# Performance work log

Hardware: AMD Instinct MI355X
Metric: run time of the kernel (lower is better)

## Reference

```python
import jax, jax.numpy as jnp
import numpy as np

B, K, N, D, E, EE, H, P = 512, 64, 1024, 128, 100000, 1024, 256, 12

def setup_inputs() -> dict:
    key = jax.random.key(0)
    ks = jax.random.split(key, 6)
    return {
        'ts_emb': jax.random.normal(ks[0], (B, D, N), jnp.float32),
        'event_table': jax.random.normal(ks[1], (E, EE), jnp.float32),
        'W_t': jax.random.normal(ks[2], (H, EE), jnp.float32) * 0.02,
        'b_t': jnp.zeros((H,), jnp.float32),
        'W_mm': jax.random.normal(ks[3], (P, H + D), jnp.float32) * 0.02,
        'b_mm': jnp.zeros((P,), jnp.float32),
        'W_ts': jax.random.normal(ks[4], (P, D), jnp.float32) * 0.02,
        'b_ts': jnp.zeros((P,), jnp.float32),
        'event_idx': jax.random.randint(ks[5], (B, K), 0, E, jnp.int64) if jax.config.read('jax_enable_x64') else jax.random.randint(ks[5], (B, K), 0, E, jnp.int32),
        'event_mask': jnp.ones((B, K), bool),
    }

def reference(ts_emb, event_table, W_t, b_t, W_mm, b_mm, W_ts, b_ts, event_idx, event_mask):
    h = W_t.shape[0]  # hidden_event_emb_dim
    # ragged event gather: [B, K, EE]
    ev = event_table[event_idx]
    # Linear(EE -> H): [B, K, H]
    ev_h = jnp.einsum('bke,he->bkh', ev, W_t) + b_t
    # masked max over events (event_fuse_type='max'): [B, H]
    neg = jnp.asarray(-jnp.inf, ev_h.dtype)
    ev_emb = jnp.max(jnp.where(event_mask[:, :, None], ev_h, neg), axis=1)
    # mm_forecaster = Conv1d(H+D -> P, k=1) on cat([event_emb repeat N, ts_emb]);
    # split the channel-wise linear so the broadcast part is never materialized.
    mm_ev = ev_emb @ W_mm[:, :h].T                       # [B, P]
    mm_ts = jnp.einsum('pd,bdn->bpn', W_mm[:, h:], ts_emb)  # [B, P, N]
    mm_pred = mm_ev[:, :, None] + mm_ts + b_mm[None, :, None]
    # ts_forecaster = Conv1d(D -> P, k=1)
    ts_pred = jnp.einsum('pd,bdn->bpn', W_ts, ts_emb) + b_ts[None, :, None]
    return (ts_pred + mm_pred) * 0.5
```

## Files before the change

kernel.cpp:

```cpp
#include <hip/hip_runtime.h>
#include <hip/hip_bf16.h>
#include <math.h>

#define B_   512
#define KEV  64
#define NN   1024
#define DD   128
#define EE_  1024
#define HH   256
#define PP   12
#define BK   128
#define NSTEP (EE_ / BK)

typedef __bf16 bf16x8 __attribute__((ext_vector_type(8)));
typedef float  f32x4  __attribute__((ext_vector_type(4)));
typedef unsigned short ushort8_t __attribute__((ext_vector_type(8)));

static __device__ __forceinline__ unsigned short f2bf(float f) {
    unsigned int u = __builtin_bit_cast(unsigned int, f);
    u = (u + 0x7FFFu + ((u >> 16) & 1u)) >> 16;
    return (unsigned short)u;
}

__global__ __launch_bounds__(256) void prep_kernel(
    const float* __restrict__ Wt,
    const float* __restrict__ Wmm,
    const float* __restrict__ Wts,
    const unsigned int* __restrict__ idxW,
    const unsigned int* __restrict__ mskW,
    unsigned short* __restrict__ WtBf,
    float* __restrict__ Wc,
    int* __restrict__ flags)
{
    if (blockIdx.x < 256) {
        int i4 = (blockIdx.x * 256 + threadIdx.x) * 4;
        const float4 v = *reinterpret_cast<const float4*>(Wt + i4);
        ushort4 o = make_ushort4(f2bf(v.x), f2bf(v.y), f2bf(v.z), f2bf(v.w));
        *reinterpret_cast<ushort4*>(WtBf + i4) = o;
        return;
    }
    __shared__ int any_nz;
    if (threadIdx.x == 0) any_nz = 0;
    __syncthreads();
    int local = 0;
    for (int k = threadIdx.x; k < (B_ * KEV) / 2; k += 256)
        local |= (idxW[2 * k + 1] != 0u);
    if (local) atomicOr(&any_nz, 1);
    for (int k = threadIdx.x; k < PP * DD; k += 256) {
        int p = k >> 7, d = k & 127;
        Wc[k] = Wmm[p * (HH + DD) + HH + d] + Wts[p * DD + d];
    }
    __syncthreads();
    if (threadIdx.x == 0) {
        flags[0] = any_nz ? 0 : 1;
        unsigned int w0 = mskW[0], w1 = mskW[1];
        flags[1] = (w0 == 0x01010101u) ? 0 : ((w1 == 0u) ? 2 : 1);
    }
}

__global__ __launch_bounds__(256, 2) void fused_kernel(
    const float* __restrict__ table,
    const void* __restrict__ idxRaw,
    const void* __restrict__ maskRaw,
    const int* __restrict__ flags,
    const unsigned short* __restrict__ WtBf,
    const float* __restrict__ bt,
    const float* __restrict__ Wmm,
    const float* __restrict__ bmm,
    const float* __restrict__ bts,
    const float* __restrict__ Wc,
    const float* __restrict__ ts,
    float* __restrict__ out)
{
    const int b = blockIdx.x;
    const int t = threadIdx.x;

    __shared__ __align__(16) unsigned short sA[2][64 * BK];
    __shared__ int           sIdx[KEV];
    __shared__ unsigned char sMask[KEV];
    __shared__ float         sEv[HH];
    __shared__ float         sC[PP];
    __shared__ float         sWc[PP * DD];

    if (t < KEV) {
        const int i = b * KEV + t;
        int id;
        if (flags[0]) id = (int)((const long long*)idxRaw)[i];
        else          id = ((const int*)idxRaw)[i];
        sIdx[t] = id;
        const int mm = flags[1];
        bool mk;
        if      (mm == 0) mk = ((const unsigned char*)maskRaw)[i] != 0;
        else if (mm == 1) mk = ((const int*)maskRaw)[i] != 0;
        else              mk = ((const long long*)maskRaw)[i] != 0;
        sMask[t] = mk ? 1 : 0;
    }
    for (int k = t; k < (PP * DD) / 4; k += 256)
        reinterpret_cast<float4*>(sWc)[k] = reinterpret_cast<const float4*>(Wc)[k];
    __syncthreads();

    const int srow  = t >> 2;
    const int seoff = (t & 3) * 32;
    const float* rowp = table + (size_t)sIdx[srow] * EE_ + seoff;

    auto loadstep = [&](int s, float4 (&r)[8]) {
        const float4* p = reinterpret_cast<const float4*>(rowp + s * BK);
        #pragma unroll
        for (int j = 0; j < 8; ++j) r[j] = p[j];
    };
    auto writebuf = [&](int bufi, const float4 (&r)[8]) {
        unsigned short* base = &sA[bufi][srow * BK];
        const int swz = ((srow & 7) << 3) ^ ((srow & 8) << 1);
        #pragma unroll
        for (int j = 0; j < 4; ++j) {
            const float4 a = r[2 * j], c = r[2 * j + 1];
            ushort8_t o;
            o[0]=f2bf(a.x); o[1]=f2bf(a.y); o[2]=f2bf(a.z); o[3]=f2bf(a.w);
            o[4]=f2bf(c.x); o[5]=f2bf(c.y); o[6]=f2bf(c.z); o[7]=f2bf(c.w);
            *reinterpret_cast<ushort8_t*>(base + ((seoff + j * 8) ^ swz)) = o;
        }
    };

    const int w    = t >> 6;
    const int lane = t & 63;
    const int lm   = lane & 15;
    const int lg   = lane >> 4;

    f32x4 acc[4][4];
    #pragma unroll
    for (int mi = 0; mi < 4; ++mi)
        #pragma unroll
        for (int ni = 0; ni < 4; ++ni)
            acc[mi][ni] = (f32x4){0.f, 0.f, 0.f, 0.f};

    const unsigned short* wtB = WtBf + (size_t)(w * 64 + lm) * EE_ + lg * 8;

    auto mfma_step = [&](int cur, int s) {
        #pragma unroll
        for (int ks = 0; ks < 4; ++ks) {
            bf16x8 af[4];
            #pragma unroll
            for (int mi = 0; mi < 4; ++mi) {
                const int row = mi * 16 + lm;
                const int e   = ks * 32 + lg * 8;
                const int es  = e ^ ((row & 7) << 3) ^ ((row & 8) << 1);
                af[mi] = *reinterpret_cast<const bf16x8*>(&sA[cur][row * BK + es]);
            }
            #pragma unroll
            for (int ni = 0; ni < 4; ++ni) {
                const unsigned short* bp = wtB + (size_t)ni * 16 * EE_ + s * BK + ks * 32;
                bf16x8 bfr = *reinterpret_cast<const bf16x8*>(bp);
                #pragma unroll
                for (int mi = 0; mi < 4; ++mi)
                    acc[mi][ni] = __builtin_amdgcn_mfma_f32_16x16x32_bf16(
                        af[mi], bfr, acc[mi][ni], 0, 0, 0);
            }
        }
    };

    float4 rA[8], rB[8];
    loadstep(0, rA);
    writebuf(0, rA);
    loadstep(1, rA);
    __syncthreads();

    #pragma unroll
    for (int ss = 0; ss < NSTEP / 2; ++ss) {
        {
            const int s = 2 * ss;
            if (s + 2 < NSTEP) loadstep(s + 2, rB);
            mfma_step(s & 1, s);
            writebuf((s + 1) & 1, rA);
            __syncthreads();
        }
        {
            const int s = 2 * ss + 1;
            if (s + 2 < NSTEP) loadstep(s + 2, rA);
            mfma_step(s & 1, s);
            if (s + 1 < NSTEP) writebuf((s + 1) & 1, rB);
            __syncthreads();
        }
    }

    #pragma unroll
    for (int ni = 0; ni < 4; ++ni) {
        float mx = -INFINITY;
        #pragma unroll
        for (int mi = 0; mi < 4; ++mi) {
            #pragma unroll
            for (int r = 0; r < 4; ++r) {
                const int ev = mi * 16 + lg * 4 + r;
                const float v = sMask[ev] ? acc[mi][ni][r] : -INFINITY;
                mx = fmaxf(mx, v);
            }
        }
        mx = fmaxf(mx, __shfl_xor(mx, 16));
        mx = fmaxf(mx, __shfl_xor(mx, 32));
        if (lg == 0) {
            const int h = w * 64 + ni * 16 + lm;
            sEv[h] = mx + bt[h];
        }
    }
    __syncthreads();

    if (w == 0) {
        #pragma unroll 1
        for (int p = 0; p < PP; ++p) {
            const float* wr = Wmm + p * (HH + DD);
            float sum = sEv[lane]       * wr[lane]
                      + sEv[lane + 64]  * wr[lane + 64]
                      + sEv[lane + 128] * wr[lane + 128]
                      + sEv[lane + 192] * wr[lane + 192];
            #pragma unroll
            for (int off = 32; off >= 1; off >>= 1) sum += __shfl_xor(sum, off);
            if (lane == 0) sC[p] = sum + bmm[p] + bts[p];
        }
    }
    __syncthreads();

    const float* tsb = ts + (size_t)b * DD * NN + t * 4;

    f32x4 tacc[PP];
    #pragma unroll
    for (int p = 0; p < PP; ++p) {
        const float c = sC[p];
        tacc[p] = (f32x4){c, c, c, c};
    }

    #pragma unroll 4
    for (int d = 0; d < DD; ++d) {
        const f32x4 v = __builtin_nontemporal_load(
            reinterpret_cast<const f32x4*>(tsb + (size_t)d * NN));
        #pragma unroll
        for (int p = 0; p < PP; ++p)
            tacc[p] += sWc[p * DD + d] * v;
    }

    float* ob = out + (size_t)b * PP * NN + t * 4;
    #pragma unroll
    for (int p = 0; p < PP; ++p) {
        const f32x4 r = tacc[p] * 0.5f;
        __builtin_nontemporal_store(r, reinterpret_cast<f32x4*>(ob + (size_t)p * NN));
    }
}

extern "C" void kernel_launch(void* const* d_in, const int* in_sizes, int n_in,
                              void* d_out, int out_size, void* d_ws, size_t ws_size,
                              hipStream_t stream)
{
    const float* ts    = (const float*)d_in[0];
    const float* table = (const float*)d_in[1];
    const float* Wt    = (const float*)d_in[2];
    const float* bt    = (const float*)d_in[3];
    const float* Wmm   = (const float*)d_in[4];
    const float* bmm   = (const float*)d_in[5];
    const float* Wts   = (const float*)d_in[6];
    const float* bts   = (const float*)d_in[7];
    const void*  idx   = (const void*)d_in[8];
    const void*  msk   = (const void*)d_in[9];
    float* out = (float*)d_out;

    unsigned short* WtBf = (unsigned short*)d_ws;
    float* Wc  = (float*)((char*)d_ws + (512u << 10));
    int*   flg = (int*)((char*)d_ws + (512u << 10) + 8192);

    prep_kernel<<<257, 256, 0, stream>>>(Wt, Wmm, Wts,
                                         (const unsigned int*)idx,
                                         (const unsigned int*)msk,
                                         WtBf, Wc, flg);
    fused_kernel<<<B_, 256, 0, stream>>>(table, idx, msk, flg, WtBf, bt,
                                         Wmm, bmm, bts, Wc, ts, out);
}
```

Measured before the change: 112.7 us.

## Interleave ts_emb projection streaming with event-gather MFMA pipeline steps

Splits the ts_emb channel projection into chunks of D/NSTEP rows and runs one chunk per event-GEMM pipeline step. The intent is to overlap the large ts_emb streaming load with the gather and MFMA phase instead of running it serially at the end. It also drops the shared-memory copy of the combined weights, reading them from global (likely scalar/cached) instead. The event pipeline becomes a non-unrolled single-register-buffer loop, which raises register pressure (tacc held live through the MFMA loop) and may lower occupancy or expose gather latency.

```diff
diff --git a/kernel.cpp b/kernel.cpp
--- a/kernel.cpp
+++ b/kernel.cpp
@@ -11,6 +11,7 @@
 #define PP   12
 #define BK   128
 #define NSTEP (EE_ / BK)
+#define TSROWS (DD / NSTEP)
 
 typedef __bf16 bf16x8 __attribute__((ext_vector_type(8)));
 typedef float  f32x4  __attribute__((ext_vector_type(4)));
@@ -80,7 +81,6 @@
     __shared__ unsigned char sMask[KEV];
     __shared__ float         sEv[HH];
     __shared__ float         sC[PP];
-    __shared__ float         sWc[PP * DD];
 
     if (t < KEV) {
         const int i = b * KEV + t;
@@ -95,8 +95,6 @@
         else              mk = ((const long long*)maskRaw)[i] != 0;
         sMask[t] = mk ? 1 : 0;
     }
-    for (int k = t; k < (PP * DD) / 4; k += 256)
-        reinterpret_cast<float4*>(sWc)[k] = reinterpret_cast<const float4*>(Wc)[k];
     __syncthreads();
 
     const int srow  = t >> 2;
@@ -132,6 +130,23 @@
         #pragma unroll
         for (int ni = 0; ni < 4; ++ni)
             acc[mi][ni] = (f32x4){0.f, 0.f, 0.f, 0.f};
+
+    const float* tsb = ts + (size_t)b * DD * NN + t * 4;
+    f32x4 tacc[PP];
+    #pragma unroll
+    for (int p = 0; p < PP; ++p) tacc[p] = (f32x4){0.f, 0.f, 0.f, 0.f};
+
+    auto ts_chunk = [&](int s) {
+        #pragma unroll 4
+        for (int j = 0; j < TSROWS; ++j) {
+            const int d = s * TSROWS + j;
+            const f32x4 v = __builtin_nontemporal_load(
+                reinterpret_cast<const f32x4*>(tsb + (size_t)d * NN));
+            #pragma unroll
+            for (int p = 0; p < PP; ++p)
+                tacc[p] += Wc[p * DD + d] * v;
+        }
+    };
 
     const unsigned short* wtB = WtBf + (size_t)(w * 64 + lm) * EE_ + lg * 8;
 
@@ -158,28 +173,18 @@
         }
     };
 
-    float4 rA[8], rB[8];
+    float4 rA[8];
     loadstep(0, rA);
     writebuf(0, rA);
-    loadstep(1, rA);
-    __syncthreads();
-
-    #pragma unroll
-    for (int ss = 0; ss < NSTEP / 2; ++ss) {
-        {
-            const int s = 2 * ss;
-            if (s + 2 < NSTEP) loadstep(s + 2, rB);
-            mfma_step(s & 1, s);
-            writebuf((s + 1) & 1, rA);
-            __syncthreads();
-        }
-        {
-            const int s = 2 * ss + 1;
-            if (s + 2 < NSTEP) loadstep(s + 2, rA);
-            mfma_step(s & 1, s);
-            if (s + 1 < NSTEP) writebuf((s + 1) & 1, rB);
-            __syncthreads();
-        }
+    __syncthreads();
+
+    #pragma unroll 1
+    for (int s = 0; s < NSTEP; ++s) {
+        if (s + 1 < NSTEP) loadstep(s + 1, rA);
+        ts_chunk(s);
+        mfma_step(s & 1, s);
+        if (s + 1 < NSTEP) writebuf((s + 1) & 1, rA);
+        __syncthreads();
     }
 
     #pragma unroll
@@ -218,28 +223,11 @@
     }
     __syncthreads();
 
-    const float* tsb = ts + (size_t)b * DD * NN + t * 4;
-
-    f32x4 tacc[PP];
+    float* ob = out + (size_t)b * PP * NN + t * 4;
     #pragma unroll
     for (int p = 0; p < PP; ++p) {
         const float c = sC[p];
-        tacc[p] = (f32x4){c, c, c, c};
-    }
-
-    #pragma unroll 4
-    for (int d = 0; d < DD; ++d) {
-        const f32x4 v = __builtin_nontemporal_load(
-            reinterpret_cast<const f32x4*>(tsb + (size_t)d * NN));
-        #pragma unroll
-        for (int p = 0; p < PP; ++p)
-            tacc[p] += sWc[p * DD + d] * v;
-    }
-
-    float* ob = out + (size_t)b * PP * NN + t * 4;
-    #pragma unroll
-    for (int p = 0; p < PP; ++p) {
-        const f32x4 r = tacc[p] * 0.5f;
+        const f32x4 r = (tacc[p] + (f32x4){c, c, c, c}) * 0.5f;
         __builtin_nontemporal_store(r, reinterpret_cast<f32x4*>(ob + (size_t)p * NN));
     }
 }
```

Result: faster. 109.0 us (-3.3%).
